# Kernel optimization log

Measured on AMD Instinct MI355X. Metric: run time of the kernel, lower is better.

Reference implementation:

```python
import jax, jax.numpy as jnp
import numpy as np

H = 16        # GRU hidden / attn embed dim
EPS = 1e-5    # BatchNorm eps


def setup_inputs() -> dict:
    key = jax.random.key(0)
    ks = jax.random.split(key, 24)
    B, T = 32768, 50
    s = 0.1
    inp = {
        "user_id": jax.random.randint(ks[0], (B,), 0, 10000),
        "history_item_id": jax.random.randint(ks[1], (B, T), 0, 10000),
        "history_category_id": jax.random.randint(ks[2], (B, T), 0, 10),
        "target_item_id": jax.random.randint(ks[3], (B, 1), 0, 10000),
        "target_category_id": jax.random.randint(ks[4], (B, 1), 0, 10),
        # embedding tables
        "user_table": jax.random.normal(ks[5], (10000, 16)) * s,
        "item_table": jax.random.normal(ks[6], (10000, 12)) * s,
        "cat_table": jax.random.normal(ks[7], (10, 4)) * s,
        # GRU (torch layout: [3H, in], gates order r,z,n)
        "gru_Wih": jax.random.normal(ks[8], (3 * H, H)) * s,
        "gru_Whh": jax.random.normal(ks[9], (3 * H, H)) * s,
        "gru_bih": jax.random.normal(ks[10], (3 * H,)) * s,
        "gru_bhh": jax.random.normal(ks[11], (3 * H,)) * s,
        # MultiheadAttention, 1 head, embed 16 (in_proj packs q,k,v)
        "mha_Win": jax.random.normal(ks[12], (3 * H, H)) * s,
        "mha_bin": jax.random.normal(ks[13], (3 * H,)) * s,
        "mha_Wout": jax.random.normal(ks[14], (H, H)) * s,
        "mha_bout": jax.random.normal(ks[15], (H,)) * s,
        # BN(48) -> Linear(48,16) -> ReLU -> BN(16) -> Linear(16,2) -> Softmax
        "bn1_g": jnp.ones((48,)),
        "bn1_b": jnp.zeros((48,)),
        "fc1_W": jax.random.normal(ks[16], (16, 48)) * s,
        "fc1_b": jax.random.normal(ks[17], (16,)) * s,
        "bn2_g": jnp.ones((16,)),
        "bn2_b": jnp.zeros((16,)),
        "fc2_W": jax.random.normal(ks[18], (2, 16)) * s,
        "fc2_b": jax.random.normal(ks[19], (2,)) * s,
    }
    return inp


def _gru(x, Wih, Whh, bih, bhh):
    # x: [B, T, H] -> outputs [B, T, H]; torch GRU cell math
    xg = jnp.einsum("bti,gi->btg", x, Wih) + bih           # [B,T,3H]
    xg = jnp.moveaxis(xg, 1, 0)                             # [T,B,3H]
    h0 = jnp.zeros((x.shape[0], H), x.dtype)

    def step(h, xt):
        hg = h @ Whh.T + bhh                                # [B,3H]
        xr, xz, xn = jnp.split(xt, 3, axis=-1)
        hr, hz, hn = jnp.split(hg, 3, axis=-1)
        r = jax.nn.sigmoid(xr + hr)
        z = jax.nn.sigmoid(xz + hz)
        n = jnp.tanh(xn + r * hn)
        h = (1.0 - z) * n + z * h
        return h, h

    _, ys = jax.lax.scan(step, h0, xg)
    return jnp.moveaxis(ys, 0, 1)                           # [B,T,H]


def _mha(q_in, kv_in, Win, bin_, Wout, bout):
    # single-head attention, batch_first
    Wq, Wk, Wv = jnp.split(Win, 3, axis=0)
    bq, bk, bv = jnp.split(bin_, 3, axis=0)
    q = q_in @ Wq.T + bq                                    # [B,T,H]
    k = kv_in @ Wk.T + bk                                   # [B,S,H]
    v = kv_in @ Wv.T + bv                                   # [B,S,H]
    scores = jnp.einsum("btd,bsd->bts", q, k) / jnp.sqrt(jnp.asarray(H, q.dtype))
    attn = jax.nn.softmax(scores, axis=-1)
    ctx = jnp.einsum("bts,bsd->btd", attn, v)
    return ctx @ Wout.T + bout                              # [B,T,H]


def _bn(x, g, b):
    # training-mode BatchNorm1d over batch axis
    mu = x.mean(axis=0)
    var = x.var(axis=0)
    return (x - mu) * jax.lax.rsqrt(var + EPS) * g + b


def reference(user_id, history_item_id, history_category_id, target_item_id,
              target_category_id, user_table, item_table, cat_table,
              gru_Wih, gru_Whh, gru_bih, gru_bhh,
              mha_Win, mha_bin, mha_Wout, mha_bout,
              bn1_g, bn1_b, fc1_W, fc1_b, bn2_g, bn2_b, fc2_W, fc2_b):
    user_emb = user_table[user_id]                          # [B,16]
    hist_emb = jnp.concatenate(
        [item_table[history_item_id], cat_table[history_category_id]], axis=-1)  # [B,T,16]
    tgt_emb = jnp.concatenate(
        [item_table[target_item_id], cat_table[target_category_id]], axis=-1)    # [B,1,16]

    hist_enc = _gru(hist_emb, gru_Wih, gru_Whh, gru_bih, gru_bhh)                 # [B,T,16]
    attn = _mha(hist_enc, tgt_emb, mha_Win, mha_bin, mha_Wout, mha_bout)          # [B,T,16]
    avg = (attn * hist_enc).sum(axis=1)                                           # [B,16]

    all_enc = jnp.concatenate([avg, tgt_emb[:, 0, :], user_emb], axis=1)          # [B,48]
    h = _bn(all_enc, bn1_g, bn1_b)
    h = jax.nn.relu(h @ fc1_W.T + fc1_b)
    h = _bn(h, bn2_g, bn2_b)
    logits = h @ fc2_W.T + fc2_b
    return jax.nn.softmax(logits, axis=-1)                                        # [B,2]
```

## Files before the change

kernel.cpp:

```cpp
#include <hip/hip_runtime.h>

#define BN_EPS 1e-5f

typedef const float* fp;
typedef float f32x4 __attribute__((ext_vector_type(4)));
typedef _Float16 f16x2 __attribute__((ext_vector_type(2)));
typedef _Float16 f16x4 __attribute__((ext_vector_type(4)));
typedef _Float16 f16x8 __attribute__((ext_vector_type(8)));

__device__ __forceinline__ float frcp(float x) { return __builtin_amdgcn_rcpf(x); }
__device__ __forceinline__ float sigm(float x) { return frcp(1.0f + __expf(-x)); }
__device__ __forceinline__ float tanh_fast(float x) { return 1.0f - 2.0f * frcp(1.0f + __expf(2.0f * x)); }

__device__ __forceinline__ f32x4 ld4(const float* p) { return *(const f32x4*)p; }
__device__ __forceinline__ float dot4(f32x4 a, f32x4 b) {
    return a[0] * b[0] + a[1] * b[1] + a[2] * b[2] + a[3] * b[3];
}

#define MFMA16(A, B, C) __builtin_amdgcn_mfma_f32_16x16x16f16((A), (B), (C), 0, 0, 0)
#define MFMA32(A, B, C) __builtin_amdgcn_mfma_f32_16x16x32_f16((A), (B), (C), 0, 0, 0)

#define GLDS16(gp, lp) __builtin_amdgcn_global_load_lds( \
    (const __attribute__((address_space(1))) void*)(gp), \
    (__attribute__((address_space(3))) void*)(lp), 16, 0, 0)

__device__ __forceinline__ f16x4 pk_f16(f32x4 v) {
    f16x2 lo = __builtin_bit_cast(f16x2, __builtin_amdgcn_cvt_pkrtz(v[0], v[1]));
    f16x2 hi = __builtin_bit_cast(f16x2, __builtin_amdgcn_cvt_pkrtz(v[2], v[3]));
    return __builtin_shufflevector(lo, hi, 0, 1, 2, 3);
}

__global__ __launch_bounds__(256) void k_precompute(
    fp Wih, fp bih, fp bhh, fp item_table, fp cat_table,
    float* __restrict__ P_item, float* __restrict__ P_cat,
    float* __restrict__ stats, int nItemElems, int nItemBlocks)
{
    __shared__ float w[768];
    for (int t = threadIdx.x; t < 768; t += blockDim.x) w[t] = Wih[t];
    __syncthreads();

    if ((int)blockIdx.x < nItemBlocks) {
        int idx = blockIdx.x * blockDim.x + threadIdx.x;
        if (idx < nItemElems) {
            int i = idx / 48, g = idx % 48;
            const float* row = item_table + (size_t)i * 12;
            float acc = 0.f;
#pragma unroll
            for (int k = 0; k < 12; ++k) acc += w[g * 16 + k] * row[k];
            P_item[idx] = acc;
        }
    } else {
        for (int t = threadIdx.x; t < 480; t += blockDim.x) {
            int c = t / 48, g = t % 48;
            float acc = bih[g] + (g < 32 ? bhh[g] : 0.f);
#pragma unroll
            for (int k = 0; k < 4; ++k) acc += w[g * 16 + 12 + k] * cat_table[c * 4 + k];
            P_cat[c * 52 + g] = acc;
        }
        if (threadIdx.x < 128) stats[threadIdx.x] = 0.f;
    }
}

__global__ __launch_bounds__(256, 2) void k_gru(
    const int* __restrict__ user_id, const int* __restrict__ hist_item,
    const int* __restrict__ hist_cat, const int* __restrict__ tgt_item,
    const int* __restrict__ tgt_cat,
    fp user_table, fp item_table, fp cat_table,
    fp Whh, fp bhh,
    fp mha_Win, fp mha_bin, fp mha_Wout, fp mha_bout,
    const float* __restrict__ P_item, const float* __restrict__ P_cat,
    float* __restrict__ all_enc, float* __restrict__ stats1, int B, int T)
{
    __shared__ float s_pcat[520];
    __shared__ float s_stage[4][2][3][256];
    __shared__ int   s_iid[4][1040];
    __shared__ int   s_cid[4][1040];
    __shared__ float lds_part[4][96];

    const int tid  = threadIdx.x;
    const int lane = tid & 63;
    const int wid  = tid >> 6;
    const int s    = lane & 15;
    const int hi   = lane >> 4;

    long b = (long)blockIdx.x * 64 + wid * 16 + s;
    const bool act = (b < B);
    if (!act) b = B - 1;

    for (int t = tid; t < 520; t += 256) s_pcat[t] = P_cat[t];

    const int ti  = tgt_item[b];
    const int tc  = tgt_cat[b];
    const int uid = user_id[b];

    {
        const int* ip = hist_item + b * T;
        const int* cp = hist_cat  + b * T;
        int* di = &s_iid[wid][s * 65];
        int* dc = &s_cid[wid][s * 65];
        for (int k = hi; k < T; k += 4) { di[k] = ip[k]; dc[k] = cp[k]; }
    }

    f32x4 wrf = ld4(&Whh[(0  + s) * 16 + 4 * hi]);
    f32x4 wzf = ld4(&Whh[(16 + s) * 16 + 4 * hi]);
    f32x4 wnf = ld4(&Whh[(32 + s) * 16 + 4 * hi]);
    f16x4 wrh = __builtin_convertvector(wrf, f16x4);
    f16x4 wzh = __builtin_convertvector(wzf, f16x4);
    f16x4 wnh = __builtin_convertvector(wnf, f16x4);
    f16x4 wrl = __builtin_convertvector(wrf - __builtin_convertvector(wrh, f32x4), f16x4);
    f16x4 wzl = __builtin_convertvector(wzf - __builtin_convertvector(wzh, f32x4), f16x4);
    f16x4 wnl = __builtin_convertvector(wnf - __builtin_convertvector(wnh, f32x4), f16x4);
    f16x8 wrA = __builtin_shufflevector(wrh, wrl, 0, 1, 2, 3, 4, 5, 6, 7);
    f16x8 wzA = __builtin_shufflevector(wzh, wzl, 0, 1, 2, 3, 4, 5, 6, 7);
    f16x8 wnA = __builtin_shufflevector(wnh, wnl, 0, 1, 2, 3, 4, 5, 6, 7);
    const f32x4 bhn4 = ld4(&bhh[32 + 4 * hi]);

    f32x4 h    = {0.f, 0.f, 0.f, 0.f};
    f32x4 hsum = {0.f, 0.f, 0.f, 0.f};
    f16x4 hh = {}, hl = {};
    const f32x4 zero4 = {0.f, 0.f, 0.f, 0.f};

    __syncthreads();

    const int T1 = T - 1;
    const int so = s * 65;
    float* stg = &s_stage[wid][0][0][0];
    const int l4 = lane * 4;

    {
        int id0 = s_iid[wid][so];
        const char* g0 = (const char*)P_item + (size_t)(unsigned)id0 * 192u + hi * 16;
        GLDS16(g0,       stg);
        GLDS16(g0 + 64,  stg + 256);
        GLDS16(g0 + 128, stg + 512);
        int i1 = (T1 >= 1) ? 1 : 0;
        int id1 = s_iid[wid][so + i1];
        const char* g1 = (const char*)P_item + (size_t)(unsigned)id1 * 192u + hi * 16;
        GLDS16(g1,       stg + 768);
        GLDS16(g1 + 64,  stg + 768 + 256);
        GLDS16(g1 + 128, stg + 768 + 512);
    }
    int cd = s_cid[wid][so];

    for (int t = 0; t < T; ++t) {
        int t2 = (t + 2 > T1) ? T1 : t + 2;
        int t1 = (t + 1 > T1) ? T1 : t + 1;
        int idn = s_iid[wid][so + t2];
        int cdn = s_cid[wid][so + t1];

        asm volatile("s_waitcnt vmcnt(3)" ::: "memory");

        float* bp = stg + (t & 1) * 768;
        f32x4 sr = ld4(bp + l4);
        f32x4 sz = ld4(bp + 256 + l4);
        f32x4 sn = ld4(bp + 512 + l4);
        const float* pcr = s_pcat + cd * 52 + 4 * hi;
        f32x4 pr = ld4(pcr), pz = ld4(pcr + 16), pn = ld4(pcr + 32);

        asm volatile("s_waitcnt lgkmcnt(0)" ::: "memory");

        const char* gn = (const char*)P_item + (size_t)(unsigned)idn * 192u + hi * 16;
        GLDS16(gn,       bp);
        GLDS16(gn + 64,  bp + 256);
        GLDS16(gn + 128, bp + 512);
        cd = cdn;

        f32x4 xr = sr + pr, xz = sz + pz, xn = sn + pn;
        f16x8 hB = __builtin_shufflevector(hh, hh, 0, 1, 2, 3, 0, 1, 2, 3);
        f32x4 aR = MFMA32(wrA, hB, xr);
        f32x4 aZ = MFMA32(wzA, hB, xz);
        f32x4 aN = MFMA32(wnA, hB, bhn4);
        f32x4 eR = MFMA16(wrh, hl, zero4);
        f32x4 eZ = MFMA16(wzh, hl, zero4);
        f32x4 eN = MFMA16(wnh, hl, zero4);
#pragma unroll
        for (int q = 0; q < 4; ++q) {
            float r = sigm(aR[q] + eR[q]);
            float z = sigm(aZ[q] + eZ[q]);
            float n = tanh_fast(fmaf(r, aN[q] + eN[q], xn[q]));
            h[q] = z * (h[q] - n) + n;
        }
        hsum += h;
        hh = pk_f16(h);
        f32x4 hb;
#pragma unroll
        for (int q = 0; q < 4; ++q) hb[q] = (float)hh[q];
        hl = pk_f16(h - hb);
    }

    const float* itr = item_table + (size_t)ti * 12;
    f32x4 tv0 = ld4(itr), tv1 = ld4(itr + 4), tv2 = ld4(itr + 8);
    f32x4 tv3 = ld4(cat_table + tc * 4);

    f32x4 vq;
#pragma unroll
    for (int q = 0; q < 4; ++q) {
        int row = 32 + 4 * hi + q;
        const float* wv = mha_Win + row * 16;
        vq[q] = mha_bin[row] + dot4(ld4(wv), tv0) + dot4(ld4(wv + 4), tv1)
              + dot4(ld4(wv + 8), tv2) + dot4(ld4(wv + 12), tv3);
    }
    f32x4 vg0, vg1, vg2, vg3;
#pragma unroll
    for (int q = 0; q < 4; ++q) {
        vg0[q] = __shfl_xor(vq[q], (hi ^ 0) << 4);
        vg1[q] = __shfl_xor(vq[q], (hi ^ 1) << 4);
        vg2[q] = __shfl_xor(vq[q], (hi ^ 2) << 4);
        vg3[q] = __shfl_xor(vq[q], (hi ^ 3) << 4);
    }
    f32x4 aj;
#pragma unroll
    for (int q = 0; q < 4; ++q) {
        int row = 4 * hi + q;
        const float* wo = mha_Wout + row * 16;
        aj[q] = mha_bout[row] + dot4(ld4(wo), vg0) + dot4(ld4(wo + 4), vg1)
              + dot4(ld4(wo + 8), vg2) + dot4(ld4(wo + 12), vg3);
    }
    f32x4 avg = aj * hsum;

    f32x4 u4 = ld4(user_table + (size_t)uid * 16 + 4 * hi);
    f32x4 t4 = (hi == 0) ? tv0 : (hi == 1) ? tv1 : (hi == 2) ? tv2 : tv3;

    if (act) {
        float* er = all_enc + b * 48 + 4 * hi;
        *(f32x4*)er        = avg;
        *(f32x4*)(er + 16) = t4;
        *(f32x4*)(er + 32) = u4;
    }

    f32x4 sa = avg, st = t4, su = u4;
    if (!act) { sa = zero4; st = zero4; su = zero4; }
    f32x4 qa = sa * sa, qt = st * st, qu = su * su;
#pragma unroll
    for (int m = 1; m <= 8; m <<= 1) {
#pragma unroll
        for (int q = 0; q < 4; ++q) {
            sa[q] += __shfl_xor(sa[q], m);
            st[q] += __shfl_xor(st[q], m);
            su[q] += __shfl_xor(su[q], m);
            qa[q] += __shfl_xor(qa[q], m);
            qt[q] += __shfl_xor(qt[q], m);
            qu[q] += __shfl_xor(qu[q], m);
        }
    }
    if (s == 0) {
        int c = 4 * hi;
#pragma unroll
        for (int q = 0; q < 4; ++q) {
            lds_part[wid][c + q]      = sa[q];
            lds_part[wid][16 + c + q] = st[q];
            lds_part[wid][32 + c + q] = su[q];
            lds_part[wid][48 + c + q] = qa[q];
            lds_part[wid][64 + c + q] = qt[q];
            lds_part[wid][80 + c + q] = qu[q];
        }
    }
    __syncthreads();
    if (tid < 96) {
        float v = lds_part[0][tid] + lds_part[1][tid] + lds_part[2][tid] + lds_part[3][tid];
        atomicAdd(&stats1[tid], v);
    }
}

__global__ __launch_bounds__(256) void k_fc1(
    const float* __restrict__ all_enc, const float* __restrict__ stats,
    fp fc1_W, fp fc1_b, fp g1, fp b1,
    float* __restrict__ hbuf, float* __restrict__ stats2, int B)
{
    const int tid = threadIdx.x, lane = tid & 63, wid = tid >> 6;
    const int j = lane & 15, sl = lane >> 4;
    __shared__ float kk[48], mm[48];
    __shared__ float part[4][32];

    if (tid < 48) {
        float mu  = stats[tid] / (float)B;
        float var = stats[48 + tid] / (float)B - mu * mu;
        float k   = rsqrtf(var + BN_EPS);
        float gk  = g1[tid] * k;
        kk[tid] = gk;
        mm[tid] = b1[tid] - mu * gk;
    }
    __syncthreads();

    float w[48];
    float bj = fc1_b[j];
#pragma unroll
    for (int q = 0; q < 12; ++q) {
        float4 v = *(const float4*)&fc1_W[j * 48 + q * 4];
        w[q * 4 + 0] = v.x * kk[q * 4 + 0];
        w[q * 4 + 1] = v.y * kk[q * 4 + 1];
        w[q * 4 + 2] = v.z * kk[q * 4 + 2];
        w[q * 4 + 3] = v.w * kk[q * 4 + 3];
        bj += v.x * mm[q * 4 + 0] + v.y * mm[q * 4 + 1]
            + v.z * mm[q * 4 + 2] + v.w * mm[q * 4 + 3];
    }

    float sh = 0.f, sq = 0.f;
    for (long b = (long)blockIdx.x * 16 + wid * 4 + sl; b < B; b += (long)gridDim.x * 16) {
        const float* x = all_enc + b * 48;
        float acc = bj;
#pragma unroll
        for (int q = 0; q < 12; ++q) {
            float4 v = *(const float4*)&x[q * 4];
            acc += w[q * 4] * v.x + w[q * 4 + 1] * v.y + w[q * 4 + 2] * v.z + w[q * 4 + 3] * v.w;
        }
        float h = fmaxf(acc, 0.f);
        hbuf[b * 16 + j] = h;
        sh += h; sq += h * h;
    }
    sh += __shfl_xor(sh, 16); sh += __shfl_xor(sh, 32);
    sq += __shfl_xor(sq, 16); sq += __shfl_xor(sq, 32);
    if (sl == 0) { part[wid][j] = sh; part[wid][16 + j] = sq; }
    __syncthreads();
    if (tid < 32) {
        float v = part[0][tid] + part[1][tid] + part[2][tid] + part[3][tid];
        atomicAdd(&stats2[tid], v);
    }
}

__global__ __launch_bounds__(256) void k_out(
    const float* __restrict__ hbuf, const float* __restrict__ stats2,
    fp fc2_W, fp fc2_b, fp g2, fp b2, float* __restrict__ out, int B)
{
    __shared__ float w[34];
    const int tid = threadIdx.x;
    if (tid < 32) {
        int c = tid & 15;
        float mu  = stats2[c] / (float)B;
        float var = stats2[16 + c] / (float)B - mu * mu;
        float gk  = g2[c] * rsqrtf(var + BN_EPS);
        w[tid] = fc2_W[tid] * gk;
    }
    if (tid < 2) {
        float acc = fc2_b[tid];
        for (int c = 0; c < 16; ++c) {
            float mu  = stats2[c] / (float)B;
            float var = stats2[16 + c] / (float)B - mu * mu;
            float gk  = g2[c] * rsqrtf(var + BN_EPS);
            acc += fc2_W[tid * 16 + c] * (b2[c] - mu * gk);
        }
        w[32 + tid] = acc;
    }
    __syncthreads();
    for (long b = (long)blockIdx.x * blockDim.x + threadIdx.x; b < B;
         b += (long)gridDim.x * blockDim.x) {
        const float* h = hbuf + b * 16;
        float l0 = w[32], l1 = w[33];
#pragma unroll
        for (int q = 0; q < 4; ++q) {
            float4 v = *(const float4*)&h[q * 4];
            l0 += w[q * 4] * v.x + w[q * 4 + 1] * v.y + w[q * 4 + 2] * v.z + w[q * 4 + 3] * v.w;
            l1 += w[16 + q * 4] * v.x + w[17 + q * 4] * v.y + w[18 + q * 4] * v.z + w[19 + q * 4] * v.w;
        }
        float m  = fmaxf(l0, l1);
        float e0 = __expf(l0 - m), e1 = __expf(l1 - m);
        float inv = frcp(e0 + e1);
        float2 p; p.x = e0 * inv; p.y = e1 * inv;
        *(float2*)&out[b * 2] = p;
    }
}

extern "C" void kernel_launch(void* const* d_in, const int* in_sizes, int n_in,
                              void* d_out, int out_size, void* d_ws, size_t ws_size,
                              hipStream_t stream)
{
    const int* user_id   = (const int*)d_in[0];
    const int* hist_item = (const int*)d_in[1];
    const int* hist_cat  = (const int*)d_in[2];
    const int* tgt_item  = (const int*)d_in[3];
    const int* tgt_cat   = (const int*)d_in[4];
    fp user_table = (fp)d_in[5];
    fp item_table = (fp)d_in[6];
    fp cat_table  = (fp)d_in[7];
    fp Wih = (fp)d_in[8],  Whh = (fp)d_in[9];
    fp bih = (fp)d_in[10], bhh = (fp)d_in[11];
    fp Win = (fp)d_in[12], binp = (fp)d_in[13];
    fp Wout = (fp)d_in[14], bout = (fp)d_in[15];
    fp g1 = (fp)d_in[16], b1 = (fp)d_in[17];
    fp fc1W = (fp)d_in[18], fc1b = (fp)d_in[19];
    fp g2 = (fp)d_in[20], b2 = (fp)d_in[21];
    fp fc2W = (fp)d_in[22], fc2b = (fp)d_in[23];

    const int B = in_sizes[0];
    const int T = in_sizes[1] / B;
    const int nItem = in_sizes[6] / 12;
    const int nItemElems = nItem * 48;

    float* ws      = (float*)d_ws;
    float* P_item  = ws;
    float* P_cat   = P_item + (size_t)nItemElems;
    float* stats   = P_cat + 520;
    float* stats2  = stats + 96;
    float* all_enc = stats + 128 + 8;
    float* hbuf    = all_enc + (size_t)B * 48;

    const int nItemBlocks = (nItemElems + 255) / 256;
    hipLaunchKernelGGL(k_precompute, dim3(nItemBlocks + 1), dim3(256), 0, stream,
                       Wih, bih, bhh, item_table, cat_table, P_item, P_cat, stats,
                       nItemElems, nItemBlocks);

    hipLaunchKernelGGL(k_gru, dim3((B + 63) / 64), dim3(256), 0, stream,
                       user_id, hist_item, hist_cat, tgt_item, tgt_cat,
                       user_table, item_table, cat_table, Whh, bhh,
                       Win, binp, Wout, bout, P_item, P_cat,
                       all_enc, stats, B, T);

    hipLaunchKernelGGL(k_fc1, dim3(512), dim3(256), 0, stream,
                       all_enc, stats, fc1W, fc1b, g1, b1, hbuf, stats2, B);

    hipLaunchKernelGGL(k_out, dim3((B + 255) / 256), dim3(256), 0, stream,
                       hbuf, stats2, fc2W, fc2b, g2, b2, (float*)d_out, B);
}
```

Baseline: 76.02 us.

## Gather padded raw item embeddings and fold input projection into GRU MFMAs

Drops the precomputed 48-wide projected item table and instead pads the raw 12-wide item embeddings to 16 floats. The GRU kernel then does the input projection in its per-step MFMAs by concatenating the embedding and hidden state in the K dimension, with hi/lo fp16 splits to keep precision. This cuts the per-step gather from three 16-byte loads to one, so the prefetch depth can grow to four steps. In exchange each step runs more MFMAs on the serial recurrence critical path, which adds latency per step.

```diff
diff --git a/kernel.cpp b/kernel.cpp
--- a/kernel.cpp
+++ b/kernel.cpp
@@ -32,29 +32,21 @@
 
 __global__ __launch_bounds__(256) void k_precompute(
     fp Wih, fp bih, fp bhh, fp item_table, fp cat_table,
-    float* __restrict__ P_item, float* __restrict__ P_cat,
-    float* __restrict__ stats, int nItemElems, int nItemBlocks)
+    float* __restrict__ itemP, float* __restrict__ P_cat,
+    float* __restrict__ stats, int nPadElems, int nPadBlocks)
 {
-    __shared__ float w[768];
-    for (int t = threadIdx.x; t < 768; t += blockDim.x) w[t] = Wih[t];
-    __syncthreads();
-
-    if ((int)blockIdx.x < nItemBlocks) {
+    if ((int)blockIdx.x < nPadBlocks) {
         int idx = blockIdx.x * blockDim.x + threadIdx.x;
-        if (idx < nItemElems) {
-            int i = idx / 48, g = idx % 48;
-            const float* row = item_table + (size_t)i * 12;
-            float acc = 0.f;
-#pragma unroll
-            for (int k = 0; k < 12; ++k) acc += w[g * 16 + k] * row[k];
-            P_item[idx] = acc;
+        if (idx < nPadElems) {
+            int i = idx >> 4, j = idx & 15;
+            itemP[idx] = (j < 12) ? item_table[i * 12 + j] : 0.f;
         }
     } else {
         for (int t = threadIdx.x; t < 480; t += blockDim.x) {
             int c = t / 48, g = t % 48;
             float acc = bih[g] + (g < 32 ? bhh[g] : 0.f);
 #pragma unroll
-            for (int k = 0; k < 4; ++k) acc += w[g * 16 + 12 + k] * cat_table[c * 4 + k];
+            for (int k = 0; k < 4; ++k) acc += Wih[g * 16 + 12 + k] * cat_table[c * 4 + k];
             P_cat[c * 52 + g] = acc;
         }
         if (threadIdx.x < 128) stats[threadIdx.x] = 0.f;
@@ -66,13 +58,13 @@
     const int* __restrict__ hist_cat, const int* __restrict__ tgt_item,
     const int* __restrict__ tgt_cat,
     fp user_table, fp item_table, fp cat_table,
-    fp Whh, fp bhh,
+    fp Whh, fp bhh, fp Wih,
     fp mha_Win, fp mha_bin, fp mha_Wout, fp mha_bout,
-    const float* __restrict__ P_item, const float* __restrict__ P_cat,
+    const float* __restrict__ itemP, const float* __restrict__ P_cat,
     float* __restrict__ all_enc, float* __restrict__ stats1, int B, int T)
 {
     __shared__ float s_pcat[520];
-    __shared__ float s_stage[4][2][3][256];
+    __shared__ float s_stage[4][4][256];
     __shared__ int   s_iid[4][1040];
     __shared__ int   s_cid[4][1040];
     __shared__ float lds_part[4][96];
@@ -101,83 +93,90 @@
         for (int k = hi; k < T; k += 4) { di[k] = ip[k]; dc[k] = cp[k]; }
     }
 
-    f32x4 wrf = ld4(&Whh[(0  + s) * 16 + 4 * hi]);
-    f32x4 wzf = ld4(&Whh[(16 + s) * 16 + 4 * hi]);
-    f32x4 wnf = ld4(&Whh[(32 + s) * 16 + 4 * hi]);
-    f16x4 wrh = __builtin_convertvector(wrf, f16x4);
-    f16x4 wzh = __builtin_convertvector(wzf, f16x4);
-    f16x4 wnh = __builtin_convertvector(wnf, f16x4);
-    f16x4 wrl = __builtin_convertvector(wrf - __builtin_convertvector(wrh, f32x4), f16x4);
-    f16x4 wzl = __builtin_convertvector(wzf - __builtin_convertvector(wzh, f32x4), f16x4);
-    f16x4 wnl = __builtin_convertvector(wnf - __builtin_convertvector(wnh, f32x4), f16x4);
-    f16x8 wrA = __builtin_shufflevector(wrh, wrl, 0, 1, 2, 3, 4, 5, 6, 7);
-    f16x8 wzA = __builtin_shufflevector(wzh, wzl, 0, 1, 2, 3, 4, 5, 6, 7);
-    f16x8 wnA = __builtin_shufflevector(wnh, wnl, 0, 1, 2, 3, 4, 5, 6, 7);
+    f32x4 whrf = ld4(&Whh[(0  + s) * 16 + 4 * hi]);
+    f32x4 whzf = ld4(&Whh[(16 + s) * 16 + 4 * hi]);
+    f32x4 whnf = ld4(&Whh[(32 + s) * 16 + 4 * hi]);
+    f32x4 wirf = ld4(&Wih[(0  + s) * 16 + 4 * hi]);
+    f32x4 wizf = ld4(&Wih[(16 + s) * 16 + 4 * hi]);
+    f32x4 winf = ld4(&Wih[(32 + s) * 16 + 4 * hi]);
+    f16x4 whr_h = __builtin_convertvector(whrf, f16x4);
+    f16x4 whz_h = __builtin_convertvector(whzf, f16x4);
+    f16x4 whn_h = __builtin_convertvector(whnf, f16x4);
+    f16x4 wir_h = __builtin_convertvector(wirf, f16x4);
+    f16x4 wiz_h = __builtin_convertvector(wizf, f16x4);
+    f16x4 win_h = __builtin_convertvector(winf, f16x4);
+    f16x4 whr_l = __builtin_convertvector(whrf - __builtin_convertvector(whr_h, f32x4), f16x4);
+    f16x4 whz_l = __builtin_convertvector(whzf - __builtin_convertvector(whz_h, f32x4), f16x4);
+    f16x4 whn_l = __builtin_convertvector(whnf - __builtin_convertvector(whn_h, f32x4), f16x4);
+    f16x4 wir_l = __builtin_convertvector(wirf - __builtin_convertvector(wir_h, f32x4), f16x4);
+    f16x4 wiz_l = __builtin_convertvector(wizf - __builtin_convertvector(wiz_h, f32x4), f16x4);
+    f16x4 win_l = __builtin_convertvector(winf - __builtin_convertvector(win_h, f32x4), f16x4);
+    f16x8 Ar  = __builtin_shufflevector(wir_h, whr_h, 0, 1, 2, 3, 4, 5, 6, 7);
+    f16x8 ArL = __builtin_shufflevector(wir_l, whr_l, 0, 1, 2, 3, 4, 5, 6, 7);
+    f16x8 Az  = __builtin_shufflevector(wiz_h, whz_h, 0, 1, 2, 3, 4, 5, 6, 7);
+    f16x8 AzL = __builtin_shufflevector(wiz_l, whz_l, 0, 1, 2, 3, 4, 5, 6, 7);
+    f16x8 Anx = __builtin_shufflevector(win_h, win_l, 0, 1, 2, 3, 4, 5, 6, 7);
+    f16x8 Anh = __builtin_shufflevector(whn_h, whn_l, 0, 1, 2, 3, 4, 5, 6, 7);
     const f32x4 bhn4 = ld4(&bhh[32 + 4 * hi]);
 
     f32x4 h    = {0.f, 0.f, 0.f, 0.f};
     f32x4 hsum = {0.f, 0.f, 0.f, 0.f};
     f16x4 hh = {}, hl = {};
-    const f32x4 zero4 = {0.f, 0.f, 0.f, 0.f};
 
     __syncthreads();
 
     const int T1 = T - 1;
     const int so = s * 65;
-    float* stg = &s_stage[wid][0][0][0];
+    float* stg = &s_stage[wid][0][0];
     const int l4 = lane * 4;
 
-    {
-        int id0 = s_iid[wid][so];
-        const char* g0 = (const char*)P_item + (size_t)(unsigned)id0 * 192u + hi * 16;
-        GLDS16(g0,       stg);
-        GLDS16(g0 + 64,  stg + 256);
-        GLDS16(g0 + 128, stg + 512);
-        int i1 = (T1 >= 1) ? 1 : 0;
-        int id1 = s_iid[wid][so + i1];
-        const char* g1 = (const char*)P_item + (size_t)(unsigned)id1 * 192u + hi * 16;
-        GLDS16(g1,       stg + 768);
-        GLDS16(g1 + 64,  stg + 768 + 256);
-        GLDS16(g1 + 128, stg + 768 + 512);
+#pragma unroll
+    for (int d = 0; d < 4; ++d) {
+        int td = (d > T1) ? T1 : d;
+        int idd = s_iid[wid][so + td];
+        GLDS16((const char*)itemP + (size_t)(unsigned)idd * 64u + hi * 16, stg + d * 256);
     }
     int cd = s_cid[wid][so];
 
     for (int t = 0; t < T; ++t) {
-        int t2 = (t + 2 > T1) ? T1 : t + 2;
+        int t4 = (t + 4 > T1) ? T1 : t + 4;
         int t1 = (t + 1 > T1) ? T1 : t + 1;
-        int idn = s_iid[wid][so + t2];
+        int idn = s_iid[wid][so + t4];
         int cdn = s_cid[wid][so + t1];
 
         asm volatile("s_waitcnt vmcnt(3)" ::: "memory");
 
-        float* bp = stg + (t & 1) * 768;
-        f32x4 sr = ld4(bp + l4);
-        f32x4 sz = ld4(bp + 256 + l4);
-        f32x4 sn = ld4(bp + 512 + l4);
-        const float* pcr = s_pcat + cd * 52 + 4 * hi;
-        f32x4 pr = ld4(pcr), pz = ld4(pcr + 16), pn = ld4(pcr + 32);
+        float* bp = stg + (t & 3) * 256;
+        f32x4 e4 = ld4(bp + l4);
+        const float* pc = s_pcat + cd * 52 + 4 * hi;
+        f32x4 pcr = ld4(pc), pcz = ld4(pc + 16), pcn = ld4(pc + 32);
 
         asm volatile("s_waitcnt lgkmcnt(0)" ::: "memory");
 
-        const char* gn = (const char*)P_item + (size_t)(unsigned)idn * 192u + hi * 16;
-        GLDS16(gn,       bp);
-        GLDS16(gn + 64,  bp + 256);
-        GLDS16(gn + 128, bp + 512);
+        GLDS16((const char*)itemP + (size_t)(unsigned)idn * 64u + hi * 16, bp);
         cd = cdn;
 
-        f32x4 xr = sr + pr, xz = sz + pz, xn = sn + pn;
-        f16x8 hB = __builtin_shufflevector(hh, hh, 0, 1, 2, 3, 0, 1, 2, 3);
-        f32x4 aR = MFMA32(wrA, hB, xr);
-        f32x4 aZ = MFMA32(wzA, hB, xz);
-        f32x4 aN = MFMA32(wnA, hB, bhn4);
-        f32x4 eR = MFMA16(wrh, hl, zero4);
-        f32x4 eZ = MFMA16(wzh, hl, zero4);
-        f32x4 eN = MFMA16(wnh, hl, zero4);
+        f16x4 e_h = pk_f16(e4);
+        f32x4 eb;
+#pragma unroll
+        for (int q = 0; q < 4; ++q) eb[q] = (float)e_h[q];
+        f16x4 e_l = pk_f16(e4 - eb);
+
+        f16x8 Bhh = __builtin_shufflevector(e_h, hh, 0, 1, 2, 3, 4, 5, 6, 7);
+        f16x8 Bll = __builtin_shufflevector(e_l, hl, 0, 1, 2, 3, 4, 5, 6, 7);
+        f16x8 Bee = __builtin_shufflevector(e_h, e_h, 0, 1, 2, 3, 0, 1, 2, 3);
+        f16x8 Bh2 = __builtin_shufflevector(hh, hh, 0, 1, 2, 3, 0, 1, 2, 3);
+
+        f32x4 aR = MFMA32(Ar, Bhh, MFMA32(Ar, Bll, MFMA32(ArL, Bhh, pcr)));
+        f32x4 aZ = MFMA32(Az, Bhh, MFMA32(Az, Bll, MFMA32(AzL, Bhh, pcz)));
+        f32x4 xn = MFMA16(win_h, e_l, MFMA32(Anx, Bee, pcn));
+        f32x4 hn = MFMA16(whn_h, hl, MFMA32(Anh, Bh2, bhn4));
+
 #pragma unroll
         for (int q = 0; q < 4; ++q) {
-            float r = sigm(aR[q] + eR[q]);
-            float z = sigm(aZ[q] + eZ[q]);
-            float n = tanh_fast(fmaf(r, aN[q] + eN[q], xn[q]));
+            float r = sigm(aR[q]);
+            float z = sigm(aZ[q]);
+            float n = tanh_fast(fmaf(r, hn[q], xn[q]));
             h[q] = z * (h[q] - n) + n;
         }
         hsum += h;
@@ -219,17 +218,17 @@
     f32x4 avg = aj * hsum;
 
     f32x4 u4 = ld4(user_table + (size_t)uid * 16 + 4 * hi);
-    f32x4 t4 = (hi == 0) ? tv0 : (hi == 1) ? tv1 : (hi == 2) ? tv2 : tv3;
+    f32x4 t4v = (hi == 0) ? tv0 : (hi == 1) ? tv1 : (hi == 2) ? tv2 : tv3;
 
     if (act) {
         float* er = all_enc + b * 48 + 4 * hi;
         *(f32x4*)er        = avg;
-        *(f32x4*)(er + 16) = t4;
+        *(f32x4*)(er + 16) = t4v;
         *(f32x4*)(er + 32) = u4;
     }
 
-    f32x4 sa = avg, st = t4, su = u4;
-    if (!act) { sa = zero4; st = zero4; su = zero4; }
+    const f32x4 zero4 = {0.f, 0.f, 0.f, 0.f};
+    f32x4 sa = act ? avg : zero4, st = act ? t4v : zero4, su = act ? u4 : zero4;
     f32x4 qa = sa * sa, qt = st * st, qu = su * su;
 #pragma unroll
     for (int m = 1; m <= 8; m <<= 1) {
@@ -384,25 +383,25 @@
     const int B = in_sizes[0];
     const int T = in_sizes[1] / B;
     const int nItem = in_sizes[6] / 12;
-    const int nItemElems = nItem * 48;
+    const int nPadElems = nItem * 16;
 
     float* ws      = (float*)d_ws;
-    float* P_item  = ws;
-    float* P_cat   = P_item + (size_t)nItemElems;
+    float* itemP   = ws;
+    float* P_cat   = itemP + (size_t)nPadElems;
     float* stats   = P_cat + 520;
     float* stats2  = stats + 96;
     float* all_enc = stats + 128 + 8;
     float* hbuf    = all_enc + (size_t)B * 48;
 
-    const int nItemBlocks = (nItemElems + 255) / 256;
-    hipLaunchKernelGGL(k_precompute, dim3(nItemBlocks + 1), dim3(256), 0, stream,
-                       Wih, bih, bhh, item_table, cat_table, P_item, P_cat, stats,
-                       nItemElems, nItemBlocks);
+    const int nPadBlocks = (nPadElems + 255) / 256;
+    hipLaunchKernelGGL(k_precompute, dim3(nPadBlocks + 1), dim3(256), 0, stream,
+                       Wih, bih, bhh, item_table, cat_table, itemP, P_cat, stats,
+                       nPadElems, nPadBlocks);
 
     hipLaunchKernelGGL(k_gru, dim3((B + 63) / 64), dim3(256), 0, stream,
                        user_id, hist_item, hist_cat, tgt_item, tgt_cat,
-                       user_table, item_table, cat_table, Whh, bhh,
-                       Win, binp, Wout, bout, P_item, P_cat,
+                       user_table, item_table, cat_table, Whh, bhh, Wih,
+                       Win, binp, Wout, bout, itemP, P_cat,
                        all_enc, stats, B, T);
 
     hipLaunchKernelGGL(k_fc1, dim3(512), dim3(256), 0, stream,
```

Result: no change. 75.59 us (-0.6%).
